# Optimization experiments

Measured on AMD Instinct MI355X. Metric: run time of the kernel, lower is better.

The kernel has to match this reference:

```python
import jax, jax.numpy as jnp
import numpy as np

N_NODES = 100000
N_EDGES = 600000
N_GRAPHS = 1024
F_IN = 32
GHC = 128
NHID = 512
NOUT = 256
N_LAYERS = 5
BN_EPS = 1e-5


def setup_inputs() -> dict:
    key = jax.random.key(0)
    ks = jax.random.split(key, 20)
    x = jax.random.normal(ks[0], (N_NODES, F_IN), dtype=jnp.float32)
    edge_index = jax.random.randint(ks[1], (2, N_EDGES), 0, N_NODES, dtype=jnp.int64)
    batch = jnp.sort(jax.random.randint(ks[2], (N_NODES,), 0, N_GRAPHS, dtype=jnp.int64))
    s = 0.05
    # layer 0 MLP (in=F_IN)
    W1_0 = jax.random.normal(ks[3], (F_IN, 2 * GHC), dtype=jnp.float32) * s
    b1_0 = jnp.zeros((2 * GHC,), jnp.float32)
    W2_0 = jax.random.normal(ks[4], (2 * GHC, GHC), dtype=jnp.float32) * s
    b2_0 = jnp.zeros((GHC,), jnp.float32)
    # layers 1..4 MLPs (in=GHC), stacked
    W1s = jax.random.normal(ks[5], (N_LAYERS - 1, GHC, 2 * GHC), dtype=jnp.float32) * s
    b1s = jnp.zeros((N_LAYERS - 1, 2 * GHC), jnp.float32)
    W2s = jax.random.normal(ks[6], (N_LAYERS - 1, 2 * GHC, GHC), dtype=jnp.float32) * s
    b2s = jnp.zeros((N_LAYERS - 1, GHC), jnp.float32)
    bn_gamma = jnp.ones((N_LAYERS, GHC), jnp.float32)
    bn_beta = jnp.zeros((N_LAYERS, GHC), jnp.float32)
    Wm1 = jax.random.normal(ks[7], (N_LAYERS * GHC, NHID), dtype=jnp.float32) * s
    bm1 = jnp.zeros((NHID,), jnp.float32)
    Wm2 = jax.random.normal(ks[8], (NHID, NOUT), dtype=jnp.float32) * s
    bm2 = jnp.zeros((NOUT,), jnp.float32)
    return dict(x=x, edge_index=edge_index, batch=batch,
                W1_0=W1_0, b1_0=b1_0, W2_0=W2_0, b2_0=b2_0,
                W1s=W1s, b1s=b1s, W2s=W2s, b2s=b2s,
                bn_gamma=bn_gamma, bn_beta=bn_beta,
                Wm1=Wm1, bm1=bm1, Wm2=Wm2, bm2=bm2)


def _gin_layer(x, src, dst, W1, b1, W2, b2, gamma, beta):
    # GINConv (eps=0): h_i = MLP(x_i + sum_{j->i} x_j)
    agg = jax.ops.segment_sum(x[src], dst, num_segments=N_NODES)
    h = x + agg
    h = jax.nn.relu(h @ W1 + b1) @ W2 + b2
    # BatchNorm1d over node dim (training-mode batch stats, biased var)
    mu = jnp.mean(h, axis=0)
    var = jnp.mean(jnp.square(h - mu), axis=0)
    h = (h - mu) * jax.lax.rsqrt(var + BN_EPS) * gamma + beta
    return jax.nn.relu(h)


def _mean_pool(x, batch):
    s = jax.ops.segment_sum(x, batch, num_segments=N_GRAPHS)
    cnt = jax.ops.segment_sum(jnp.ones((x.shape[0],), x.dtype), batch, num_segments=N_GRAPHS)
    return s / jnp.maximum(cnt, 1.0)[:, None]


def reference(x, edge_index, batch, W1_0, b1_0, W2_0, b2_0,
              W1s, b1s, W2s, b2s, bn_gamma, bn_beta, Wm1, bm1, Wm2, bm2):
    src, dst = edge_index[0], edge_index[1]
    xs = []
    h = _gin_layer(x, src, dst, W1_0, b1_0, W2_0, b2_0, bn_gamma[0], bn_beta[0])
    xs.append(_mean_pool(h, batch))
    for l in range(N_LAYERS - 1):  # fixed, structurally distinct params per layer
        h = _gin_layer(h, src, dst, W1s[l], b1s[l], W2s[l], b2s[l],
                       bn_gamma[l + 1], bn_beta[l + 1])
        xs.append(_mean_pool(h, batch))
    z = jnp.concatenate(xs, axis=1)  # [G, 5*GHC]
    z = jax.nn.relu(z @ Wm1 + bm1)
    return z @ Wm2 + bm2  # [G, NOUT]
```

## Files before the change

### kernel.cpp

```cpp
#include <hip/hip_runtime.h>

#define N_NODES 100000
#define N_EDGES 600000
#define N_GRAPHS 1024
#define F_IN 32
#define GHC 128
#define NHID 512
#define NOUT 256
#define N_LAYERS 5
#define BN_EPS 1e-5f

typedef __attribute__((ext_vector_type(4))) float f32x4;
typedef __attribute__((ext_vector_type(8))) short bf16x8;

__device__ __forceinline__ unsigned short f2bf(float f) {
    unsigned int u = __float_as_uint(f);
    u = u + 0x7fffu + ((u >> 16) & 1u);
    return (unsigned short)(u >> 16);
}
__device__ __forceinline__ float bf2f(unsigned short h) {
    return __uint_as_float(((unsigned int)h) << 16);
}
__device__ __forceinline__ void load_lds16(const void* g, void* l) {
    __builtin_amdgcn_global_load_lds((const __attribute__((address_space(1))) void*)g,
                                     (__attribute__((address_space(3))) void*)l, 16, 0, 0);
}

__global__ void deg_kernel(const int* __restrict__ dst, int* __restrict__ deg) {
    int e = blockIdx.x * blockDim.x + threadIdx.x;
    if (e < N_EDGES) atomicAdd(&deg[dst[e]], 1);
}

#define SCHUNK 1024
#define NCHUNKS ((N_NODES + SCHUNK - 1) / SCHUNK)

__global__ __launch_bounds__(1024)
void scan1_kernel(const int* __restrict__ deg, int* __restrict__ ptr, int* __restrict__ btot) {
    __shared__ int buf[SCHUNK];
    int t = threadIdx.x;
    int i = blockIdx.x * SCHUNK + t;
    int v = (i < N_NODES) ? deg[i] : 0;
    buf[t] = v;
    __syncthreads();
    for (int off = 1; off < SCHUNK; off <<= 1) {
        int u = (t >= off) ? buf[t - off] : 0;
        __syncthreads();
        buf[t] += u;
        __syncthreads();
    }
    if (i < N_NODES) ptr[i + 1] = buf[t];
    if (t == SCHUNK - 1) btot[blockIdx.x] = buf[t];
}

__global__ __launch_bounds__(128)
void scan2_kernel(int* __restrict__ btot) {
    __shared__ int buf[128];
    int t = threadIdx.x;
    int v = (t < NCHUNKS) ? btot[t] : 0;
    buf[t] = v;
    __syncthreads();
    for (int off = 1; off < 128; off <<= 1) {
        int u = (t >= off) ? buf[t - off] : 0;
        __syncthreads();
        buf[t] += u;
        __syncthreads();
    }
    if (t < NCHUNKS) btot[t] = buf[t] - v;
}

__global__ void scan3_kernel(int* __restrict__ ptr, const int* __restrict__ btot) {
    int i = blockIdx.x * blockDim.x + threadIdx.x;
    if (i < N_NODES) ptr[i + 1] += btot[i >> 10];
    if (i == 0) ptr[0] = 0;
}

__global__ void fill_kernel(const int* __restrict__ src, const int* __restrict__ dst,
                            int* __restrict__ cur, int* __restrict__ adj) {
    int e = blockIdx.x * blockDim.x + threadIdx.x;
    if (e >= N_EDGES) return;
    int p = atomicAdd(&cur[dst[e]], 1);
    adj[p] = src[e];
}

__global__ void gptr_kernel(const int* __restrict__ batch, int* __restrict__ gptr) {
    int g = blockIdx.x * blockDim.x + threadIdx.x;
    if (g > N_GRAPHS) return;
    int lo = 0, hi = N_NODES;
    while (lo < hi) { int mid = (lo + hi) >> 1; if (batch[mid] < g) lo = mid + 1; else hi = mid; }
    gptr[g] = lo;
}

__global__ void wconv_kernel(const float* __restrict__ W, unsigned short* __restrict__ thi,
                             unsigned short* __restrict__ tlo, int K, int N) {
    int i = blockIdx.x * blockDim.x + threadIdx.x;
    if (i >= K * N) return;
    int k = i / N, n = i - k * N;
    float v = W[i];
    unsigned short h = f2bf(v);
    thi[(size_t)n * K + k] = h;
    tlo[(size_t)n * K + k] = f2bf(v - bf2f(h));
}

template<int F>
__global__ __launch_bounds__(256)
void gather_agg_kernel(const float* __restrict__ x, const int* __restrict__ ptr,
                       const int* __restrict__ adj,
                       unsigned short* __restrict__ ahi, unsigned short* __restrict__ alo) {
    constexpr int F4 = F / 4;
    constexpr int NPB = 256 / F4;
    int f4 = threadIdx.x % F4;
    int n = blockIdx.x * NPB + threadIdx.x / F4;
    if (n >= N_NODES) return;
    const int fo = f4 * 4;
    float4 acc = *(const float4*)(x + (size_t)n * F + fo);
    int p1 = ptr[n + 1];
    for (int p = ptr[n]; p < p1; ++p) {
        int s = adj[p];
        float4 v = *(const float4*)(x + (size_t)s * F + fo);
        acc.x += v.x; acc.y += v.y; acc.z += v.z; acc.w += v.w;
    }
    ushort4 h4, l4;
    h4.x = f2bf(acc.x); l4.x = f2bf(acc.x - bf2f(h4.x));
    h4.y = f2bf(acc.y); l4.y = f2bf(acc.y - bf2f(h4.y));
    h4.z = f2bf(acc.z); l4.z = f2bf(acc.z - bf2f(h4.z));
    h4.w = f2bf(acc.w); l4.w = f2bf(acc.w - bf2f(h4.w));
    *(ushort4*)(ahi + (size_t)n * F + fo) = h4;
    *(ushort4*)(alo + (size_t)n * F + fo) = l4;
}

__global__ __launch_bounds__(512)
void fused_mlp_kernel(const unsigned short* __restrict__ Ahi, const unsigned short* __restrict__ Alo,
                      const unsigned short* __restrict__ W1hi, const unsigned short* __restrict__ W1lo,
                      const unsigned short* __restrict__ W2hi, const unsigned short* __restrict__ W2lo,
                      const float* __restrict__ b1, const float* __restrict__ b2,
                      float* __restrict__ Of, float* __restrict__ bnsums,
                      int M, int K)
{
    __shared__ __align__(16) unsigned short AsL[2][4][128][8];
    __shared__ __align__(16) unsigned short hidL[2][32][128][8];
    __shared__ float sred[GHC], qred[GHC];

    const int tid = threadIdx.x;
    const int wv = tid >> 6, lane = tid & 63;
    const int r = lane & 15, g = lane >> 4;
    const int row0 = blockIdx.x * 128;

    if (tid < GHC) { sred[tid] = 0.f; qred[tid] = 0.f; }

    const int wm = wv >> 2, wn = wv & 3;
    f32x4 acc[4][4];
#pragma unroll
    for (int mi = 0; mi < 4; ++mi)
#pragma unroll
        for (int ni = 0; ni < 4; ++ni) acc[mi][ni] = 0.f;

    const int srow = tid & 127, skg = tid >> 7;
    int arow = row0 + srow; if (arow >= M) arow = M - 1;
    unsigned short* dA0 = &AsL[0][0][0][0] + wv * 512;
    unsigned short* dA1 = &AsL[1][0][0][0] + wv * 512;

    for (int k0 = 0; k0 < K; k0 += 32) {
        const size_t aoff = (size_t)arow * K + k0 + skg * 8;
        load_lds16(Ahi + aoff, dA0);
        load_lds16(Alo + aoff, dA1);
        __syncthreads();
        bf16x8 ah[4], al[4], bh[4], bl[4];
#pragma unroll
        for (int i = 0; i < 4; ++i) {
            const int ar = wm * 64 + i * 16 + r;
            ah[i] = *(const bf16x8*)&AsL[0][g][ar][0];
            al[i] = *(const bf16x8*)&AsL[1][g][ar][0];
            const int n1 = wn * 64 + i * 16 + r;
            const size_t w1off = (size_t)n1 * K + k0 + g * 8;
            bh[i] = *(const bf16x8*)(W1hi + w1off);
            bl[i] = *(const bf16x8*)(W1lo + w1off);
        }
#pragma unroll
        for (int mi = 0; mi < 4; ++mi)
#pragma unroll
            for (int ni = 0; ni < 4; ++ni) {
                acc[mi][ni] = __builtin_amdgcn_mfma_f32_16x16x32_bf16(ah[mi], bh[ni], acc[mi][ni], 0, 0, 0);
                acc[mi][ni] = __builtin_amdgcn_mfma_f32_16x16x32_bf16(ah[mi], bl[ni], acc[mi][ni], 0, 0, 0);
                acc[mi][ni] = __builtin_amdgcn_mfma_f32_16x16x32_bf16(al[mi], bh[ni], acc[mi][ni], 0, 0, 0);
            }
        __syncthreads();
    }
#pragma unroll
    for (int ni = 0; ni < 4; ++ni) {
        const int n1 = wn * 64 + ni * 16 + r;
        const float bb = b1[n1];
#pragma unroll
        for (int mi = 0; mi < 4; ++mi)
#pragma unroll
            for (int reg = 0; reg < 4; ++reg) {
                const int lrow = wm * 64 + mi * 16 + g * 4 + reg;
                float v = fmaxf(acc[mi][ni][reg] + bb, 0.f);
                unsigned short h = f2bf(v);
                hidL[0][n1 >> 3][lrow][n1 & 7] = h;
                hidL[1][n1 >> 3][lrow][n1 & 7] = f2bf(v - bf2f(h));
            }
    }
    __syncthreads();

    const int wk = wv >> 2, t2 = wv & 3, wm2 = t2 >> 1, wn2 = t2 & 1;
#pragma unroll
    for (int mi = 0; mi < 4; ++mi)
#pragma unroll
        for (int ni = 0; ni < 4; ++ni) acc[mi][ni] = 0.f;

    const int kb = wk * 128;
#pragma unroll
    for (int s = 0; s < 4; ++s) {
        const int k0 = kb + s * 32;
        bf16x8 a2h[4], a2l[4], b2h[4], b2l[4];
#pragma unroll
        for (int i = 0; i < 4; ++i) {
            const int ar = wm2 * 64 + i * 16 + r;
            a2h[i] = *(const bf16x8*)&hidL[0][(k0 >> 3) + g][ar][0];
            a2l[i] = *(const bf16x8*)&hidL[1][(k0 >> 3) + g][ar][0];
            const int n2 = wn2 * 64 + i * 16 + r;
            const size_t w2off = (size_t)n2 * 256 + k0 + g * 8;
            b2h[i] = *(const bf16x8*)(W2hi + w2off);
            b2l[i] = *(const bf16x8*)(W2lo + w2off);
        }
#pragma unroll
        for (int mi = 0; mi < 4; ++mi)
#pragma unroll
            for (int ni = 0; ni < 4; ++ni) {
                acc[mi][ni] = __builtin_amdgcn_mfma_f32_16x16x32_bf16(a2h[mi], b2h[ni], acc[mi][ni], 0, 0, 0);
                acc[mi][ni] = __builtin_amdgcn_mfma_f32_16x16x32_bf16(a2h[mi], b2l[ni], acc[mi][ni], 0, 0, 0);
                acc[mi][ni] = __builtin_amdgcn_mfma_f32_16x16x32_bf16(a2l[mi], b2h[ni], acc[mi][ni], 0, 0, 0);
            }
    }
    __syncthreads();

    float* scr = (float*)&hidL[0][0][0][0];
    if (wk == 1) {
#pragma unroll
        for (int mi = 0; mi < 4; ++mi)
#pragma unroll
            for (int ni = 0; ni < 4; ++ni)
                *(f32x4*)&scr[((t2 * 64 + ni * 16 + r) * 68 + mi * 16 + g * 4)] = acc[mi][ni];
    }
    __syncthreads();
    if (wk == 0) {
        float sl[4] = {0.f, 0.f, 0.f, 0.f}, ql[4] = {0.f, 0.f, 0.f, 0.f};
#pragma unroll
        for (int ni = 0; ni < 4; ++ni) {
            const int n2 = wn2 * 64 + ni * 16 + r;
            const float bb = b2[n2];
#pragma unroll
            for (int mi = 0; mi < 4; ++mi) {
                f32x4 p = *(const f32x4*)&scr[((t2 * 64 + ni * 16 + r) * 68 + mi * 16 + g * 4)];
#pragma unroll
                for (int reg = 0; reg < 4; ++reg) {
                    const int grow = row0 + wm2 * 64 + mi * 16 + g * 4 + reg;
                    if (grow < M) {
                        float v = acc[mi][ni][reg] + p[reg] + bb;
                        Of[(size_t)grow * GHC + n2] = v;
                        sl[ni] += v; ql[ni] += v * v;
                    }
                }
            }
        }
#pragma unroll
        for (int ni = 0; ni < 4; ++ni) {
            const int n2 = wn2 * 64 + ni * 16 + r;
            atomicAdd(&sred[n2], sl[ni]);
            atomicAdd(&qred[n2], ql[ni]);
        }
    }
    __syncthreads();
    if (tid < GHC) {
        atomicAdd(&bnsums[tid], sred[tid]);
        atomicAdd(&bnsums[GHC + tid], qred[tid]);
    }
}

__global__ void bn_finalize_kernel(const float* __restrict__ sums,
    const float* __restrict__ gamma, const float* __restrict__ beta,
    float* __restrict__ ss) {
    int f = threadIdx.x;
    if (f < GHC) {
        float mu = sums[f] * (1.f / N_NODES);
        float var = sums[GHC + f] * (1.f / N_NODES) - mu * mu;
        float sc = gamma[f] * rsqrtf(var + BN_EPS);
        ss[f] = sc;
        ss[GHC + f] = beta[f] - mu * sc;
    }
}

__global__ __launch_bounds__(256)
void bn_apply_kernel(const float* __restrict__ h2, const float* __restrict__ ss,
                     float* __restrict__ hout) {
    int idx = blockIdx.x * blockDim.x + threadIdx.x;
    int node = idx >> 5;
    if (node >= N_NODES) return;
    int f = (idx & 31) * 4;
    float4 v = *(const float4*)(h2 + (size_t)node * GHC + f);
    float4 sc = *(const float4*)(ss + f);
    float4 sh = *(const float4*)(ss + GHC + f);
    float4 o;
    o.x = fmaxf(v.x * sc.x + sh.x, 0.f);
    o.y = fmaxf(v.y * sc.y + sh.y, 0.f);
    o.z = fmaxf(v.z * sc.z + sh.z, 0.f);
    o.w = fmaxf(v.w * sc.w + sh.w, 0.f);
    *(float4*)(hout + (size_t)node * GHC + f) = o;
}

__global__ __launch_bounds__(128)
void pool_kernel(const float* __restrict__ h, const int* __restrict__ gptr,
                 float* __restrict__ z, int loff) {
    int g = blockIdx.x;
    int f = threadIdx.x;
    int s = gptr[g], e = gptr[g + 1];
    float acc = 0.f;
    for (int i = s; i < e; ++i) acc += h[(size_t)i * GHC + f];
    z[(size_t)g * (N_LAYERS * GHC) + loff + f] = acc / fmaxf((float)(e - s), 1.f);
}

template<bool RELU>
__global__ __launch_bounds__(256)
void gemm64_kernel(const float* __restrict__ A, const float* __restrict__ W,
                   const float* __restrict__ bias, float* __restrict__ C,
                   int M, int K, int N) {
    __shared__ float As[16][68];
    __shared__ float Bs[16][64];
    const int tid = threadIdx.x;
    const int row0 = blockIdx.x * 64;
    const int col0 = blockIdx.y * 64;
    const int tx = tid & 15;
    const int ty = tid >> 4;
    const int lm = tid >> 2;
    const int lk = (tid & 3) * 4;
    const int bkr = tid >> 4;
    const int bnc = (tid & 15) * 4;

    float acc[4][4];
#pragma unroll
    for (int i = 0; i < 4; ++i)
#pragma unroll
        for (int j = 0; j < 4; ++j) acc[i][j] = 0.f;

    const int arow = row0 + lm;
    for (int k0 = 0; k0 < K; k0 += 16) {
        if (arow < M) {
            float4 v = *(const float4*)(A + (size_t)arow * K + k0 + lk);
            As[lk + 0][lm] = v.x; As[lk + 1][lm] = v.y;
            As[lk + 2][lm] = v.z; As[lk + 3][lm] = v.w;
        } else {
#pragma unroll
            for (int j = 0; j < 4; ++j) As[lk + j][lm] = 0.f;
        }
        *(float4*)&Bs[bkr][bnc] = *(const float4*)(W + (size_t)(k0 + bkr) * N + col0 + bnc);
        __syncthreads();
#pragma unroll
        for (int kk = 0; kk < 16; ++kk) {
            float a[4], b[4];
            *(float4*)&a[0] = *(const float4*)&As[kk][ty * 4];
            *(float4*)&b[0] = *(const float4*)&Bs[kk][tx * 4];
#pragma unroll
            for (int i = 0; i < 4; ++i)
#pragma unroll
                for (int j = 0; j < 4; ++j)
                    acc[i][j] = fmaf(a[i], b[j], acc[i][j]);
        }
        __syncthreads();
    }
    float4 bv = *(const float4*)(bias + col0 + tx * 4);
    float bb[4] = {bv.x, bv.y, bv.z, bv.w};
#pragma unroll
    for (int i = 0; i < 4; ++i) {
        int row = row0 + ty * 4 + i;
        if (row < M) {
            float o[4];
#pragma unroll
            for (int j = 0; j < 4; ++j) {
                float t = acc[i][j] + bb[j];
                o[j] = RELU ? fmaxf(t, 0.f) : t;
            }
            *(float4*)(C + (size_t)row * N + col0 + tx * 4) = *(float4*)&o[0];
        }
    }
}

extern "C" void kernel_launch(void* const* d_in, const int* in_sizes, int n_in,
                              void* d_out, int out_size, void* d_ws, size_t ws_size,
                              hipStream_t stream)
{
    const float* x = (const float*)d_in[0];
    const int* edge = (const int*)d_in[1];
    const int* batch = (const int*)d_in[2];
    const float* W1_0 = (const float*)d_in[3];
    const float* b1_0 = (const float*)d_in[4];
    const float* W2_0 = (const float*)d_in[5];
    const float* b2_0 = (const float*)d_in[6];
    const float* W1s = (const float*)d_in[7];
    const float* b1s = (const float*)d_in[8];
    const float* W2s = (const float*)d_in[9];
    const float* b2s = (const float*)d_in[10];
    const float* gamma = (const float*)d_in[11];
    const float* beta = (const float*)d_in[12];
    const float* Wm1 = (const float*)d_in[13];
    const float* bm1 = (const float*)d_in[14];
    const float* Wm2 = (const float*)d_in[15];
    const float* bm2 = (const float*)d_in[16];
    const int* srcI = edge;
    const int* dstI = edge + N_EDGES;

    unsigned short* agg_hi = (unsigned short*)d_ws;
    unsigned short* agg_lo = agg_hi + (size_t)N_NODES * GHC;
    float* h2 = (float*)(agg_lo + (size_t)N_NODES * GHC);
    float* hbuf = h2 + (size_t)N_NODES * GHC;
    float* z = hbuf + (size_t)N_NODES * GHC;
    float* zh = z + (size_t)N_GRAPHS * N_LAYERS * GHC;
    float* bnsums = zh + (size_t)N_GRAPHS * NHID;
    float* bnss = bnsums + 2 * GHC;
    unsigned short* w1t_hi = (unsigned short*)(bnss + 2 * GHC);
    unsigned short* w1t_lo = w1t_hi + 256 * GHC;
    unsigned short* w2t_hi = w1t_lo + 256 * GHC;
    unsigned short* w2t_lo = w2t_hi + 256 * GHC;
    int* ideg = (int*)(w2t_lo + 256 * GHC);
    int* iptr = ideg + N_NODES;
    int* iadj = iptr + N_NODES + 1;
    int* ibtot = iadj + N_EDGES;
    int* igptr = ibtot + 128;

    hipMemsetAsync(ideg, 0, N_NODES * sizeof(int), stream);
    deg_kernel<<<(N_EDGES + 255) / 256, 256, 0, stream>>>(dstI, ideg);
    scan1_kernel<<<NCHUNKS, SCHUNK, 0, stream>>>(ideg, iptr, ibtot);
    scan2_kernel<<<1, 128, 0, stream>>>(ibtot);
    scan3_kernel<<<(N_NODES + 255) / 256, 256, 0, stream>>>(iptr, ibtot);
    hipMemcpyAsync(ideg, iptr, N_NODES * sizeof(int), hipMemcpyDeviceToDevice, stream);
    fill_kernel<<<(N_EDGES + 255) / 256, 256, 0, stream>>>(srcI, dstI, ideg, iadj);
    gptr_kernel<<<(N_GRAPHS + 1 + 255) / 256, 256, 0, stream>>>(batch, igptr);

    const int MB = (N_NODES + 127) / 128;
    const float* hin = x;
    for (int l = 0; l < N_LAYERS; ++l) {
        const int F = (l == 0) ? F_IN : GHC;
        const float* W1 = (l == 0) ? W1_0 : W1s + (size_t)(l - 1) * GHC * 2 * GHC;
        const float* b1 = (l == 0) ? b1_0 : b1s + (size_t)(l - 1) * 2 * GHC;
        const float* W2 = (l == 0) ? W2_0 : W2s + (size_t)(l - 1) * 2 * GHC * GHC;
        const float* b2 = (l == 0) ? b2_0 : b2s + (size_t)(l - 1) * GHC;

        wconv_kernel<<<(F * 2 * GHC + 255) / 256, 256, 0, stream>>>(W1, w1t_hi, w1t_lo, F, 2 * GHC);
        wconv_kernel<<<(2 * GHC * GHC + 255) / 256, 256, 0, stream>>>(W2, w2t_hi, w2t_lo, 2 * GHC, GHC);

        if (l == 0)
            gather_agg_kernel<F_IN><<<(N_NODES + 31) / 32, 256, 0, stream>>>(hin, iptr, iadj, agg_hi, agg_lo);
        else
            gather_agg_kernel<GHC><<<(N_NODES + 7) / 8, 256, 0, stream>>>(hin, iptr, iadj, agg_hi, agg_lo);

        hipMemsetAsync(bnsums, 0, sizeof(float) * 2 * GHC, stream);
        fused_mlp_kernel<<<MB, 512, 0, stream>>>(agg_hi, agg_lo, w1t_hi, w1t_lo, w2t_hi, w2t_lo,
                                                 b1, b2, h2, bnsums, N_NODES, F);

        bn_finalize_kernel<<<1, GHC, 0, stream>>>(bnsums, gamma + l * GHC, beta + l * GHC, bnss);
        bn_apply_kernel<<<(N_NODES * 32 + 255) / 256, 256, 0, stream>>>(h2, bnss, hbuf);
        pool_kernel<<<N_GRAPHS, 128, 0, stream>>>(hbuf, igptr, z, l * GHC);

        hin = hbuf;
    }

    dim3 gh1(N_GRAPHS / 64, NHID / 64);
    gemm64_kernel<true><<<gh1, 256, 0, stream>>>(z, Wm1, bm1, zh, N_GRAPHS, N_LAYERS * GHC, NHID);
    dim3 gh2(N_GRAPHS / 64, NOUT / 64);
    gemm64_kernel<false><<<gh2, 256, 0, stream>>>(zh, Wm2, bm2, (float*)d_out, N_GRAPHS, NHID, NOUT);
}
```

Before: 1.476 ms.

## Fold BN-apply into gather and pool, restructure fused MLP to 256 threads

Removes the separate bn_apply kernel and its hbuf write by applying the BatchNorm scale/shift and ReLU inside the neighbour gather and the mean-pool kernels, reading raw h2 directly. The fused MLP kernel is restructured to 4 waves that process the 256-wide hidden layer in two 128-column halves, with a smaller LDS footprint and A loaded straight from global memory instead of staged through LDS. The goal is to save a full N×128 read/write pass per layer and to allow two blocks per CU. In exchange, the gather now redoes the BN arithmetic once per edge, and the MLP drops its LDS staging of A and reloads A for each hidden half.

After: 1.342 ms. 9.0% less time.

```diff
diff --git a/kernel.cpp b/kernel.cpp
--- a/kernel.cpp
+++ b/kernel.cpp
@@ -20,10 +20,6 @@
 }
 __device__ __forceinline__ float bf2f(unsigned short h) {
     return __uint_as_float(((unsigned int)h) << 16);
-}
-__device__ __forceinline__ void load_lds16(const void* g, void* l) {
-    __builtin_amdgcn_global_load_lds((const __attribute__((address_space(1))) void*)g,
-                                     (__attribute__((address_space(3))) void*)l, 16, 0, 0);
 }
 
 __global__ void deg_kernel(const int* __restrict__ dst, int* __restrict__ deg) {
@@ -101,10 +97,10 @@
     tlo[(size_t)n * K + k] = f2bf(v - bf2f(h));
 }
 
-template<int F>
+template<int F, bool BN>
 __global__ __launch_bounds__(256)
 void gather_agg_kernel(const float* __restrict__ x, const int* __restrict__ ptr,
-                       const int* __restrict__ adj,
+                       const int* __restrict__ adj, const float* __restrict__ ss,
                        unsigned short* __restrict__ ahi, unsigned short* __restrict__ alo) {
     constexpr int F4 = F / 4;
     constexpr int NPB = 256 / F4;
@@ -112,11 +108,21 @@
     int n = blockIdx.x * NPB + threadIdx.x / F4;
     if (n >= N_NODES) return;
     const int fo = f4 * 4;
+    float4 sc, sh;
+    if (BN) { sc = *(const float4*)(ss + fo); sh = *(const float4*)(ss + GHC + fo); }
     float4 acc = *(const float4*)(x + (size_t)n * F + fo);
+    if (BN) {
+        acc.x = fmaxf(acc.x * sc.x + sh.x, 0.f); acc.y = fmaxf(acc.y * sc.y + sh.y, 0.f);
+        acc.z = fmaxf(acc.z * sc.z + sh.z, 0.f); acc.w = fmaxf(acc.w * sc.w + sh.w, 0.f);
+    }
     int p1 = ptr[n + 1];
     for (int p = ptr[n]; p < p1; ++p) {
         int s = adj[p];
         float4 v = *(const float4*)(x + (size_t)s * F + fo);
+        if (BN) {
+            v.x = fmaxf(v.x * sc.x + sh.x, 0.f); v.y = fmaxf(v.y * sc.y + sh.y, 0.f);
+            v.z = fmaxf(v.z * sc.z + sh.z, 0.f); v.w = fmaxf(v.w * sc.w + sh.w, 0.f);
+        }
         acc.x += v.x; acc.y += v.y; acc.z += v.z; acc.w += v.w;
     }
     ushort4 h4, l4;
@@ -128,7 +134,7 @@
     *(ushort4*)(alo + (size_t)n * F + fo) = l4;
 }
 
-__global__ __launch_bounds__(512)
+__global__ __launch_bounds__(256, 2)
 void fused_mlp_kernel(const unsigned short* __restrict__ Ahi, const unsigned short* __restrict__ Alo,
                       const unsigned short* __restrict__ W1hi, const unsigned short* __restrict__ W1lo,
                       const unsigned short* __restrict__ W2hi, const unsigned short* __restrict__ W2lo,
@@ -136,139 +142,122 @@
                       float* __restrict__ Of, float* __restrict__ bnsums,
                       int M, int K)
 {
-    __shared__ __align__(16) unsigned short AsL[2][4][128][8];
-    __shared__ __align__(16) unsigned short hidL[2][32][128][8];
+    __shared__ __align__(16) unsigned short hidL[2][16][128][8];
     __shared__ float sred[GHC], qred[GHC];
 
     const int tid = threadIdx.x;
     const int wv = tid >> 6, lane = tid & 63;
     const int r = lane & 15, g = lane >> 4;
+    const int wm = wv >> 1, wn = wv & 1;
     const int row0 = blockIdx.x * 128;
 
     if (tid < GHC) { sred[tid] = 0.f; qred[tid] = 0.f; }
 
-    const int wm = wv >> 2, wn = wv & 3;
-    f32x4 acc[4][4];
+    int arows[4];
+#pragma unroll
+    for (int i = 0; i < 4; ++i) {
+        int rr = row0 + wm * 64 + i * 16 + r;
+        arows[i] = rr < M ? rr : M - 1;
+    }
+
+    f32x4 acc2[4][4];
 #pragma unroll
     for (int mi = 0; mi < 4; ++mi)
 #pragma unroll
-        for (int ni = 0; ni < 4; ++ni) acc[mi][ni] = 0.f;
-
-    const int srow = tid & 127, skg = tid >> 7;
-    int arow = row0 + srow; if (arow >= M) arow = M - 1;
-    unsigned short* dA0 = &AsL[0][0][0][0] + wv * 512;
-    unsigned short* dA1 = &AsL[1][0][0][0] + wv * 512;
-
-    for (int k0 = 0; k0 < K; k0 += 32) {
-        const size_t aoff = (size_t)arow * K + k0 + skg * 8;
-        load_lds16(Ahi + aoff, dA0);
-        load_lds16(Alo + aoff, dA1);
-        __syncthreads();
-        bf16x8 ah[4], al[4], bh[4], bl[4];
-#pragma unroll
-        for (int i = 0; i < 4; ++i) {
-            const int ar = wm * 64 + i * 16 + r;
-            ah[i] = *(const bf16x8*)&AsL[0][g][ar][0];
-            al[i] = *(const bf16x8*)&AsL[1][g][ar][0];
-            const int n1 = wn * 64 + i * 16 + r;
-            const size_t w1off = (size_t)n1 * K + k0 + g * 8;
-            bh[i] = *(const bf16x8*)(W1hi + w1off);
-            bl[i] = *(const bf16x8*)(W1lo + w1off);
-        }
+        for (int ni = 0; ni < 4; ++ni) acc2[mi][ni] = 0.f;
+
+#pragma unroll
+    for (int hh = 0; hh < 2; ++hh) {
+        f32x4 acc1[4][4];
 #pragma unroll
         for (int mi = 0; mi < 4; ++mi)
 #pragma unroll
-            for (int ni = 0; ni < 4; ++ni) {
-                acc[mi][ni] = __builtin_amdgcn_mfma_f32_16x16x32_bf16(ah[mi], bh[ni], acc[mi][ni], 0, 0, 0);
-                acc[mi][ni] = __builtin_amdgcn_mfma_f32_16x16x32_bf16(ah[mi], bl[ni], acc[mi][ni], 0, 0, 0);
-                acc[mi][ni] = __builtin_amdgcn_mfma_f32_16x16x32_bf16(al[mi], bh[ni], acc[mi][ni], 0, 0, 0);
+            for (int ni = 0; ni < 4; ++ni) acc1[mi][ni] = 0.f;
+
+        for (int k0 = 0; k0 < K; k0 += 32) {
+            bf16x8 ah[4], al[4], bh[4], bl[4];
+#pragma unroll
+            for (int i = 0; i < 4; ++i) {
+                const size_t ao = (size_t)arows[i] * K + k0 + g * 8;
+                ah[i] = *(const bf16x8*)(Ahi + ao);
+                al[i] = *(const bf16x8*)(Alo + ao);
+                const int n1g = hh * 128 + wn * 64 + i * 16 + r;
+                const size_t wo = (size_t)n1g * K + k0 + g * 8;
+                bh[i] = *(const bf16x8*)(W1hi + wo);
+                bl[i] = *(const bf16x8*)(W1lo + wo);
             }
-        __syncthreads();
-    }
+#pragma unroll
+            for (int mi = 0; mi < 4; ++mi)
+#pragma unroll
+                for (int ni = 0; ni < 4; ++ni) {
+                    acc1[mi][ni] = __builtin_amdgcn_mfma_f32_16x16x32_bf16(ah[mi], bh[ni], acc1[mi][ni], 0, 0, 0);
+                    acc1[mi][ni] = __builtin_amdgcn_mfma_f32_16x16x32_bf16(ah[mi], bl[ni], acc1[mi][ni], 0, 0, 0);
+                    acc1[mi][ni] = __builtin_amdgcn_mfma_f32_16x16x32_bf16(al[mi], bh[ni], acc1[mi][ni], 0, 0, 0);
+                }
+        }
+        __syncthreads();
+#pragma unroll
+        for (int ni = 0; ni < 4; ++ni) {
+            const int n1 = wn * 64 + ni * 16 + r;
+            const float bb = b1[hh * 128 + n1];
+#pragma unroll
+            for (int mi = 0; mi < 4; ++mi)
+#pragma unroll
+                for (int reg = 0; reg < 4; ++reg) {
+                    const int lrow = wm * 64 + mi * 16 + g * 4 + reg;
+                    float v = fmaxf(acc1[mi][ni][reg] + bb, 0.f);
+                    unsigned short h = f2bf(v);
+                    hidL[0][n1 >> 3][lrow][n1 & 7] = h;
+                    hidL[1][n1 >> 3][lrow][n1 & 7] = f2bf(v - bf2f(h));
+                }
+        }
+        __syncthreads();
+#pragma unroll
+        for (int s = 0; s < 4; ++s) {
+            bf16x8 a2h[4], a2l[4], b2h[4], b2l[4];
+#pragma unroll
+            for (int i = 0; i < 4; ++i) {
+                const int ar = wm * 64 + i * 16 + r;
+                a2h[i] = *(const bf16x8*)&hidL[0][s * 4 + g][ar][0];
+                a2l[i] = *(const bf16x8*)&hidL[1][s * 4 + g][ar][0];
+                const int n2 = wn * 64 + i * 16 + r;
+                const size_t wo2 = (size_t)n2 * 256 + hh * 128 + s * 32 + g * 8;
+                b2h[i] = *(const bf16x8*)(W2hi + wo2);
+                b2l[i] = *(const bf16x8*)(W2lo + wo2);
+            }
+#pragma unroll
+            for (int mi = 0; mi < 4; ++mi)
+#pragma unroll
+                for (int ni = 0; ni < 4; ++ni) {
+                    acc2[mi][ni] = __builtin_amdgcn_mfma_f32_16x16x32_bf16(a2h[mi], b2h[ni], acc2[mi][ni], 0, 0, 0);
+                    acc2[mi][ni] = __builtin_amdgcn_mfma_f32_16x16x32_bf16(a2h[mi], b2l[ni], acc2[mi][ni], 0, 0, 0);
+                    acc2[mi][ni] = __builtin_amdgcn_mfma_f32_16x16x32_bf16(a2l[mi], b2h[ni], acc2[mi][ni], 0, 0, 0);
+                }
+        }
+    }
+
+    float sl[4] = {0.f, 0.f, 0.f, 0.f}, ql[4] = {0.f, 0.f, 0.f, 0.f};
 #pragma unroll
     for (int ni = 0; ni < 4; ++ni) {
-        const int n1 = wn * 64 + ni * 16 + r;
-        const float bb = b1[n1];
+        const int n2 = wn * 64 + ni * 16 + r;
+        const float bb = b2[n2];
 #pragma unroll
         for (int mi = 0; mi < 4; ++mi)
 #pragma unroll
             for (int reg = 0; reg < 4; ++reg) {
-                const int lrow = wm * 64 + mi * 16 + g * 4 + reg;
-                float v = fmaxf(acc[mi][ni][reg] + bb, 0.f);
-                unsigned short h = f2bf(v);
-                hidL[0][n1 >> 3][lrow][n1 & 7] = h;
-                hidL[1][n1 >> 3][lrow][n1 & 7] = f2bf(v - bf2f(h));
-            }
-    }
-    __syncthreads();
-
-    const int wk = wv >> 2, t2 = wv & 3, wm2 = t2 >> 1, wn2 = t2 & 1;
-#pragma unroll
-    for (int mi = 0; mi < 4; ++mi)
-#pragma unroll
-        for (int ni = 0; ni < 4; ++ni) acc[mi][ni] = 0.f;
-
-    const int kb = wk * 128;
-#pragma unroll
-    for (int s = 0; s < 4; ++s) {
-        const int k0 = kb + s * 32;
-        bf16x8 a2h[4], a2l[4], b2h[4], b2l[4];
-#pragma unroll
-        for (int i = 0; i < 4; ++i) {
-            const int ar = wm2 * 64 + i * 16 + r;
-            a2h[i] = *(const bf16x8*)&hidL[0][(k0 >> 3) + g][ar][0];
-            a2l[i] = *(const bf16x8*)&hidL[1][(k0 >> 3) + g][ar][0];
-            const int n2 = wn2 * 64 + i * 16 + r;
-            const size_t w2off = (size_t)n2 * 256 + k0 + g * 8;
-            b2h[i] = *(const bf16x8*)(W2hi + w2off);
-            b2l[i] = *(const bf16x8*)(W2lo + w2off);
-        }
-#pragma unroll
-        for (int mi = 0; mi < 4; ++mi)
-#pragma unroll
-            for (int ni = 0; ni < 4; ++ni) {
-                acc[mi][ni] = __builtin_amdgcn_mfma_f32_16x16x32_bf16(a2h[mi], b2h[ni], acc[mi][ni], 0, 0, 0);
-                acc[mi][ni] = __builtin_amdgcn_mfma_f32_16x16x32_bf16(a2h[mi], b2l[ni], acc[mi][ni], 0, 0, 0);
-                acc[mi][ni] = __builtin_amdgcn_mfma_f32_16x16x32_bf16(a2l[mi], b2h[ni], acc[mi][ni], 0, 0, 0);
-            }
-    }
-    __syncthreads();
-
-    float* scr = (float*)&hidL[0][0][0][0];
-    if (wk == 1) {
-#pragma unroll
-        for (int mi = 0; mi < 4; ++mi)
-#pragma unroll
-            for (int ni = 0; ni < 4; ++ni)
-                *(f32x4*)&scr[((t2 * 64 + ni * 16 + r) * 68 + mi * 16 + g * 4)] = acc[mi][ni];
-    }
-    __syncthreads();
-    if (wk == 0) {
-        float sl[4] = {0.f, 0.f, 0.f, 0.f}, ql[4] = {0.f, 0.f, 0.f, 0.f};
-#pragma unroll
-        for (int ni = 0; ni < 4; ++ni) {
-            const int n2 = wn2 * 64 + ni * 16 + r;
-            const float bb = b2[n2];
-#pragma unroll
-            for (int mi = 0; mi < 4; ++mi) {
-                f32x4 p = *(const f32x4*)&scr[((t2 * 64 + ni * 16 + r) * 68 + mi * 16 + g * 4)];
-#pragma unroll
-                for (int reg = 0; reg < 4; ++reg) {
-                    const int grow = row0 + wm2 * 64 + mi * 16 + g * 4 + reg;
-                    if (grow < M) {
-                        float v = acc[mi][ni][reg] + p[reg] + bb;
-                        Of[(size_t)grow * GHC + n2] = v;
-                        sl[ni] += v; ql[ni] += v * v;
-                    }
+                const int grow = row0 + wm * 64 + mi * 16 + g * 4 + reg;
+                if (grow < M) {
+                    float v = acc2[mi][ni][reg] + bb;
+                    Of[(size_t)grow * GHC + n2] = v;
+                    sl[ni] += v; ql[ni] += v * v;
                 }
             }
-        }
-#pragma unroll
-        for (int ni = 0; ni < 4; ++ni) {
-            const int n2 = wn2 * 64 + ni * 16 + r;
-            atomicAdd(&sred[n2], sl[ni]);
-            atomicAdd(&qred[n2], ql[ni]);
-        }
+    }
+#pragma unroll
+    for (int ni = 0; ni < 4; ++ni) {
+        const int n2 = wn * 64 + ni * 16 + r;
+        atomicAdd(&sred[n2], sl[ni]);
+        atomicAdd(&qred[n2], ql[ni]);
     }
     __syncthreads();
     if (tid < GHC) {
@@ -290,32 +279,15 @@
     }
 }
 
-__global__ __launch_bounds__(256)
-void bn_apply_kernel(const float* __restrict__ h2, const float* __restrict__ ss,
-                     float* __restrict__ hout) {
-    int idx = blockIdx.x * blockDim.x + threadIdx.x;
-    int node = idx >> 5;
-    if (node >= N_NODES) return;
-    int f = (idx & 31) * 4;
-    float4 v = *(const float4*)(h2 + (size_t)node * GHC + f);
-    float4 sc = *(const float4*)(ss + f);
-    float4 sh = *(const float4*)(ss + GHC + f);
-    float4 o;
-    o.x = fmaxf(v.x * sc.x + sh.x, 0.f);
-    o.y = fmaxf(v.y * sc.y + sh.y, 0.f);
-    o.z = fmaxf(v.z * sc.z + sh.z, 0.f);
-    o.w = fmaxf(v.w * sc.w + sh.w, 0.f);
-    *(float4*)(hout + (size_t)node * GHC + f) = o;
-}
-
 __global__ __launch_bounds__(128)
-void pool_kernel(const float* __restrict__ h, const int* __restrict__ gptr,
-                 float* __restrict__ z, int loff) {
+void pool_kernel(const float* __restrict__ h2, const float* __restrict__ ss,
+                 const int* __restrict__ gptr, float* __restrict__ z, int loff) {
     int g = blockIdx.x;
     int f = threadIdx.x;
+    float sc = ss[f], sh = ss[GHC + f];
     int s = gptr[g], e = gptr[g + 1];
     float acc = 0.f;
-    for (int i = s; i < e; ++i) acc += h[(size_t)i * GHC + f];
+    for (int i = s; i < e; ++i) acc += fmaxf(h2[(size_t)i * GHC + f] * sc + sh, 0.f);
     z[(size_t)g * (N_LAYERS * GHC) + loff + f] = acc / fmaxf((float)(e - s), 1.f);
 }
 
@@ -411,8 +383,7 @@
     unsigned short* agg_hi = (unsigned short*)d_ws;
     unsigned short* agg_lo = agg_hi + (size_t)N_NODES * GHC;
     float* h2 = (float*)(agg_lo + (size_t)N_NODES * GHC);
-    float* hbuf = h2 + (size_t)N_NODES * GHC;
-    float* z = hbuf + (size_t)N_NODES * GHC;
+    float* z = h2 + (size_t)N_NODES * GHC;
     float* zh = z + (size_t)N_GRAPHS * N_LAYERS * GHC;
     float* bnsums = zh + (size_t)N_GRAPHS * NHID;
     float* bnss = bnsums + 2 * GHC;
@@ -436,7 +407,6 @@
     gptr_kernel<<<(N_GRAPHS + 1 + 255) / 256, 256, 0, stream>>>(batch, igptr);
 
     const int MB = (N_NODES + 127) / 128;
-    const float* hin = x;
     for (int l = 0; l < N_LAYERS; ++l) {
         const int F = (l == 0) ? F_IN : GHC;
         const float* W1 = (l == 0) ? W1_0 : W1s + (size_t)(l - 1) * GHC * 2 * GHC;
@@ -448,19 +418,16 @@
         wconv_kernel<<<(2 * GHC * GHC + 255) / 256, 256, 0, stream>>>(W2, w2t_hi, w2t_lo, 2 * GHC, GHC);
 
         if (l == 0)
-            gather_agg_kernel<F_IN><<<(N_NODES + 31) / 32, 256, 0, stream>>>(hin, iptr, iadj, agg_hi, agg_lo);
+            gather_agg_kernel<F_IN, false><<<(N_NODES + 31) / 32, 256, 0, stream>>>(x, iptr, iadj, nullptr, agg_hi, agg_lo);
         else
-            gather_agg_kernel<GHC><<<(N_NODES + 7) / 8, 256, 0, stream>>>(hin, iptr, iadj, agg_hi, agg_lo);
+            gather_agg_kernel<GHC, true><<<(N_NODES + 7) / 8, 256, 0, stream>>>(h2, iptr, iadj, bnss, agg_hi, agg_lo);
 
         hipMemsetAsync(bnsums, 0, sizeof(float) * 2 * GHC, stream);
-        fused_mlp_kernel<<<MB, 512, 0, stream>>>(agg_hi, agg_lo, w1t_hi, w1t_lo, w2t_hi, w2t_lo,
+        fused_mlp_kernel<<<MB, 256, 0, stream>>>(agg_hi, agg_lo, w1t_hi, w1t_lo, w2t_hi, w2t_lo,
                                                  b1, b2, h2, bnsums, N_NODES, F);
 
         bn_finalize_kernel<<<1, GHC, 0, stream>>>(bnsums, gamma + l * GHC, beta + l * GHC, bnss);
-        bn_apply_kernel<<<(N_NODES * 32 + 255) / 256, 256, 0, stream>>>(h2, bnss, hbuf);
-        pool_kernel<<<N_GRAPHS, 128, 0, stream>>>(hbuf, igptr, z, l * GHC);
-
-        hin = hbuf;
+        pool_kernel<<<N_GRAPHS, 128, 0, stream>>>(h2, bnss, igptr, z, l * GHC);
     }
 
     dim3 gh1(N_GRAPHS / 64, NHID / 64);
```
